# Kernel optimization log

Hardware: AMD Instinct MI355X
Metric: run time of the kernel (lower is better)

The kernel has to match this reference:

```python
import jax, jax.numpy as jnp
import numpy as np

B, T, C, H = 4096, 4, 1024, 8
DH = C // H
SCALE = DH ** -0.5
LN_EPS = 1e-5


def setup_inputs() -> dict:
    key = jax.random.key(0)
    k1, k2, k3 = jax.random.split(key, 3)
    feats = jax.random.normal(k1, (B, T, C), dtype=jnp.float32)
    Wqkv = jax.random.normal(k2, (T, C, 3 * C), dtype=jnp.float32) * 0.02
    bqkv = jnp.zeros((T, 3 * C), dtype=jnp.float32)
    Wproj = jax.random.normal(k3, (T, C, C), dtype=jnp.float32) * 0.02
    bproj = jnp.zeros((T, C), dtype=jnp.float32)
    gamma = jnp.ones((C,), dtype=jnp.float32)
    beta = jnp.zeros((C,), dtype=jnp.float32)
    return {"feats": feats, "Wqkv": Wqkv, "bqkv": bqkv,
            "Wproj": Wproj, "bproj": bproj, "gamma": gamma, "beta": beta}


def reference(feats, Wqkv, bqkv, Wproj, bproj, gamma, beta):
    # Grouped per-task QKV projection: [B,T,C] x [T,C,3C] -> [B,T,3C]
    qkv = jnp.einsum('btc,tcd->btd', feats, Wqkv) + bqkv
    q, k, v = jnp.split(qkv, 3, axis=-1)           # each [B,T,C]
    q = q.reshape(B, T, H, DH)
    k = k.reshape(B, T, H, DH)
    v = v.reshape(B, T, H, DH)
    # Cross-task attention: scores[b, query_task, key_task, head]
    scores = jnp.einsum('bqhd,bkhd->bqkh', q, k) * SCALE
    attn = jax.nn.softmax(scores, axis=2)          # softmax over key-task dim
    ctx = jnp.einsum('bqkh,bkhd->bqhd', attn, v)   # [B,T,H,DH]
    ctx = ctx.reshape(B, T, C)
    # Grouped per-task output projection (dropout is identity in eval)
    ctx = jnp.einsum('btc,tcd->btd', ctx, Wproj) + bproj
    # Residual + shared LayerNorm over channel dim
    x = ctx + feats
    mu = jnp.mean(x, axis=-1, keepdims=True)
    var = jnp.mean(jnp.square(x - mu), axis=-1, keepdims=True)
    return (x - mu) * jax.lax.rsqrt(var + LN_EPS) * gamma + beta
```

## Files before the change

kernel.cpp:

```cpp
#include <hip/hip_runtime.h>
#include <hip/hip_bf16.h>
#include <cstdint>
#include <cstddef>

#define B_SZ 4096
#define T_SZ 4
#define C_SZ 1024
#define H_SZ 8
#define DH_SZ 128
#define NQKV 3072
#define SCALE_F 0.08838834764831845f

typedef float f32x4 __attribute__((ext_vector_type(4)));
typedef short s16x8 __attribute__((ext_vector_type(8)));

static __device__ __forceinline__ float bf2f(unsigned short u) {
    union { unsigned int i; float f; } x; x.i = ((unsigned int)u) << 16; return x.f;
}
static __device__ __forceinline__ unsigned short f2bf(float f) {
    union { unsigned int i; float f; } x; x.f = f;
    unsigned int r = x.i + 0x7FFFu + ((x.i >> 16) & 1u);
    return (unsigned short)(r >> 16);
}

typedef const __attribute__((address_space(1))) void* gas_ptr;
typedef __attribute__((address_space(3))) void* las_ptr;
static __device__ __forceinline__ void async16(const void* g, void* l) {
    __builtin_amdgcn_global_load_lds((gas_ptr)g, (las_ptr)l, 16, 0, 0);
}

__global__ __launch_bounds__(256) void cvt_f32_bf16(const float* __restrict__ src,
                                                    unsigned short* __restrict__ dst, int n4) {
    int i = blockIdx.x * 256 + threadIdx.x;
    if (i >= n4) return;
    float4 v = reinterpret_cast<const float4*>(src)[i];
    ushort4 o;
    o.x = f2bf(v.x); o.y = f2bf(v.y); o.z = f2bf(v.z); o.w = f2bf(v.w);
    reinterpret_cast<ushort4*>(dst)[i] = o;
}

__global__ __launch_bounds__(256) void transpose_cvt(const float* __restrict__ src,
                                                     unsigned short* __restrict__ dst,
                                                     int K, int N) {
    __shared__ float tile[32][33];
    const float* s = src + (size_t)blockIdx.z * K * N;
    unsigned short* d = dst + (size_t)blockIdx.z * K * N;
    int n0 = blockIdx.x * 32, k0 = blockIdx.y * 32;
    int tx = threadIdx.x, ty = threadIdx.y;
#pragma unroll
    for (int i = 0; i < 4; i++) {
        int k = k0 + ty + i * 8;
        tile[ty + i * 8][tx] = s[(size_t)k * N + n0 + tx];
    }
    __syncthreads();
#pragma unroll
    for (int i = 0; i < 4; i++) {
        int n = n0 + ty + i * 8;
        d[(size_t)n * K + k0 + tx] = f2bf(tile[tx][ty + i * 8]);
    }
}

template<int NSIZE, int EPI>
__global__ __launch_bounds__(512, 1) void gemm256(
    const unsigned short* __restrict__ A,
    const unsigned short* __restrict__ Bt,
    const float* __restrict__ bias,
    const float* __restrict__ resid,
    unsigned short* __restrict__ out_bf,
    float* __restrict__ out_f)
{
    constexpr int BK  = 64;
    constexpr int NBX = NSIZE / 256;
    constexpr int NBY = B_SZ / 256;
    constexpr int NWG = NBX * NBY * T_SZ;

    __shared__ __align__(16) unsigned short lds[65536];

    const int bid = blockIdx.x;
    const int swz = (bid & 7) * (NWG >> 3) + (bid >> 3);
    const int by  = swz & (NBY - 1);
    const int tmp = swz >> 4;
    const int bx  = tmp % NBX;
    const int t   = tmp / NBX;
    const int m0  = by * 256;
    const int n0  = bx * 256;

    const int tid  = threadIdx.x;
    const int lane = tid & 63;
    const int w    = tid >> 6;
    const int wm   = w >> 2;
    const int wn   = w & 3;
    const int quad = lane >> 4;
    const int l16  = lane & 15;

    const int q0  = w * 128 + lane;
    const int q1  = q0 + 64;
    const int r0  = q0 >> 3, ch0 = (q0 & 7) ^ (r0 & 7);
    const int r1  = q1 >> 3, ch1 = (q1 & 7) ^ (r1 & 7);
    const unsigned short* Abase = A + (size_t)t * C_SZ;
    const unsigned short* Bbase = Bt + (size_t)t * NSIZE * C_SZ;
    const unsigned short* gA0 = Abase + (size_t)(m0 + r0) * (T_SZ * C_SZ) + ch0 * 8;
    const unsigned short* gA1 = Abase + (size_t)(m0 + r1) * (T_SZ * C_SZ) + ch1 * 8;
    const unsigned short* gB0 = Bbase + (size_t)(n0 + r0) * C_SZ + ch0 * 8;
    const unsigned short* gB1 = Bbase + (size_t)(n0 + r1) * C_SZ + ch1 * 8;
    unsigned short* dA0 = &lds[(w * 2 + 0) * 512];
    unsigned short* dA1 = &lds[(w * 2 + 1) * 512];
    unsigned short* dB0 = &lds[32768 + (w * 2 + 0) * 512];
    unsigned short* dB1 = &lds[32768 + (w * 2 + 1) * 512];

#define STG_A(buf, h, kt) do { \
    async16(gA0 + (size_t)(h) * 128 * (T_SZ * C_SZ) + (kt) * BK, dA0 + (buf) * 16384 + (h) * 8192); \
    async16(gA1 + (size_t)(h) * 128 * (T_SZ * C_SZ) + (kt) * BK, dA1 + (buf) * 16384 + (h) * 8192); \
} while (0)
#define STG_B(buf, h, kt) do { \
    async16(gB0 + (size_t)(h) * 128 * C_SZ + (kt) * BK, dB0 + (buf) * 16384 + (h) * 8192); \
    async16(gB1 + (size_t)(h) * 128 * C_SZ + (kt) * BK, dB1 + (buf) * 16384 + (h) * 8192); \
} while (0)

    const int s7   = l16 & 7;
    const int swk0 = ((0 * 4 + quad) ^ s7) * 8;
    const int swk1 = ((1 * 4 + quad) ^ s7) * 8;
    const unsigned short* aR = &lds[wm * 8192 + l16 * 64];
    const unsigned short* bR = &lds[32768 + (wn >> 1) * 8192 + ((wn & 1) * 64 + l16) * 64];

#define LD_A(buf, mh) do { \
    _Pragma("unroll") \
    for (int mi = 0; mi < 4; ++mi) { \
        af[mi][0] = *(const s16x8*)(aR + (buf) * 16384 + ((mh) * 4 + mi) * 1024 + swk0); \
        af[mi][1] = *(const s16x8*)(aR + (buf) * 16384 + ((mh) * 4 + mi) * 1024 + swk1); \
    } \
} while (0)
#define LD_B(buf, nh, dst) do { \
    _Pragma("unroll") \
    for (int ni = 0; ni < 2; ++ni) { \
        dst[ni][0] = *(const s16x8*)(bR + (buf) * 16384 + ((nh) * 2 + ni) * 1024 + swk0); \
        dst[ni][1] = *(const s16x8*)(bR + (buf) * 16384 + ((nh) * 2 + ni) * 1024 + swk1); \
    } \
} while (0)
#define MM(mh, nh, bsrc) do { \
    _Pragma("unroll") \
    for (int mi = 0; mi < 4; ++mi) \
    _Pragma("unroll") \
    for (int ni = 0; ni < 2; ++ni) { \
        acc[(mh) * 4 + mi][(nh) * 2 + ni] = __builtin_amdgcn_mfma_f32_16x16x32_bf16( \
            af[mi][0], bsrc[ni][0], acc[(mh) * 4 + mi][(nh) * 2 + ni], 0, 0, 0); \
        acc[(mh) * 4 + mi][(nh) * 2 + ni] = __builtin_amdgcn_mfma_f32_16x16x32_bf16( \
            af[mi][1], bsrc[ni][1], acc[(mh) * 4 + mi][(nh) * 2 + ni], 0, 0, 0); \
    } \
} while (0)
#define WAITK() do { \
    asm volatile("s_waitcnt lgkmcnt(0)"); \
    __builtin_amdgcn_sched_barrier(0); \
} while (0)
#define KTILE(buf, kt, SP0, SP23, VMC) do { \
     \
    asm volatile("s_waitcnt vmcnt(" #VMC ")"); \
    __builtin_amdgcn_sched_barrier(0); \
    __builtin_amdgcn_s_barrier(); \
    LD_A(buf, 0); LD_B(buf, 0, bq0); \
    if (SP0) STG_A((buf) ^ 1, 1, (kt) + 1); \
    WAITK(); \
    __builtin_amdgcn_s_setprio(1); MM(0, 0, bq0); __builtin_amdgcn_s_setprio(0); \
     \
    __builtin_amdgcn_s_barrier(); \
    LD_B(buf, 1, bq1); \
    WAITK(); \
    __builtin_amdgcn_s_setprio(1); MM(0, 1, bq1); __builtin_amdgcn_s_setprio(0); \
     \
    __builtin_amdgcn_s_barrier(); \
    LD_A(buf, 1); \
    if (SP23) { STG_B(buf, 0, (kt) + 2); STG_B(buf, 1, (kt) + 2); } \
    WAITK(); \
    __builtin_amdgcn_s_setprio(1); MM(1, 1, bq1); __builtin_amdgcn_s_setprio(0); \
     \
    __builtin_amdgcn_s_barrier(); \
    if (SP23) STG_A(buf, 0, (kt) + 2); \
    __builtin_amdgcn_s_setprio(1); MM(1, 0, bq0); __builtin_amdgcn_s_setprio(0); \
} while (0)

    f32x4 acc[8][4] = {};
    s16x8 af[4][2], bq0[2][2], bq1[2][2];

    STG_B(0, 0, 0); STG_B(0, 1, 0); STG_A(0, 0, 0); STG_A(0, 1, 0);
    STG_B(1, 0, 1); STG_B(1, 1, 1); STG_A(1, 0, 1);

#pragma clang loop unroll(disable)
    for (int it = 0; it < 7; ++it) {
        int kt = it * 2;
        KTILE(0, kt, 1, 1, 6);
        KTILE(1, kt + 1, 1, 1, 6);
    }
    KTILE(0, 14, 1, 0, 6);
    KTILE(1, 15, 0, 0, 0);

#undef KTILE
#undef WAITK
#undef MM
#undef LD_B
#undef LD_A
#undef STG_B
#undef STG_A

#pragma unroll
    for (int ni = 0; ni < 4; ++ni) {
        int gn = n0 + wn * 64 + ni * 16 + l16;
        float bi = bias[t * NSIZE + gn];
#pragma unroll
        for (int mi = 0; mi < 8; ++mi) {
#pragma unroll
            for (int r = 0; r < 4; ++r) {
                int gm = m0 + wm * 128 + mi * 16 + quad * 4 + r;
                size_t o = (size_t)(gm * T_SZ + t) * NSIZE + gn;
                float v = acc[mi][ni][r] + bi;
                if (EPI == 0) {
                    out_bf[o] = f2bf(v);
                } else {
                    out_f[o] = v + resid[o];
                }
            }
        }
    }
}

__global__ __launch_bounds__(256) void attn_kernel(const unsigned short* __restrict__ qkv,
                                                   unsigned short* __restrict__ ctx) {
    const int tid = threadIdx.x;
    const int li  = tid & 15;
    const int g   = blockIdx.x * 16 + (tid >> 4);
    const int b   = g >> 3, h = g & 7;
    const int d0  = li * 8;

    const unsigned short* base = qkv + (size_t)b * (T_SZ * NQKV) + h * DH_SZ + d0;
    float qf[4][8], kf[4][8], vf[4][8];
#pragma unroll
    for (int i = 0; i < 4; i++) {
        const unsigned short* p = base + (size_t)i * NQKV;
        s16x8 qv = *reinterpret_cast<const s16x8*>(p);
        s16x8 kv = *reinterpret_cast<const s16x8*>(p + C_SZ);
        s16x8 vv = *reinterpret_cast<const s16x8*>(p + 2 * C_SZ);
#pragma unroll
        for (int e = 0; e < 8; e++) {
            qf[i][e] = bf2f((unsigned short)qv[e]);
            kf[i][e] = bf2f((unsigned short)kv[e]);
            vf[i][e] = bf2f((unsigned short)vv[e]);
        }
    }
    float s[4][4];
#pragma unroll
    for (int i = 0; i < 4; i++)
#pragma unroll
        for (int j = 0; j < 4; j++) {
            float p = 0.0f;
#pragma unroll
            for (int e = 0; e < 8; e++) p += qf[i][e] * kf[j][e];
            p += __shfl_xor(p, 8);
            p += __shfl_xor(p, 4);
            p += __shfl_xor(p, 2);
            p += __shfl_xor(p, 1);
            s[i][j] = p * SCALE_F;
        }
#pragma unroll
    for (int i = 0; i < 4; i++) {
        float m = fmaxf(fmaxf(s[i][0], s[i][1]), fmaxf(s[i][2], s[i][3]));
        float e0 = __expf(s[i][0] - m), e1 = __expf(s[i][1] - m);
        float e2 = __expf(s[i][2] - m), e3 = __expf(s[i][3] - m);
        float inv = 1.0f / (e0 + e1 + e2 + e3);
        s[i][0] = e0 * inv; s[i][1] = e1 * inv; s[i][2] = e2 * inv; s[i][3] = e3 * inv;
    }
#pragma unroll
    for (int i = 0; i < 4; i++) {
        s16x8 ov;
#pragma unroll
        for (int e = 0; e < 8; e++) {
            float o = s[i][0] * vf[0][e] + s[i][1] * vf[1][e]
                    + s[i][2] * vf[2][e] + s[i][3] * vf[3][e];
            ov[e] = (short)f2bf(o);
        }
        *reinterpret_cast<s16x8*>(ctx + (size_t)(b * T_SZ + i) * C_SZ + h * DH_SZ + d0) = ov;
    }
}

__global__ __launch_bounds__(256) void ln_kernel(const float* __restrict__ y,
                                                 const float* __restrict__ gamma,
                                                 const float* __restrict__ beta,
                                                 float* __restrict__ out) {
    int row = blockIdx.x;
    int lane = threadIdx.x & 63, wave = threadIdx.x >> 6;
    float4 v = reinterpret_cast<const float4*>(y + (size_t)row * C_SZ)[threadIdx.x];
    float s  = v.x + v.y + v.z + v.w;
    float ss = v.x * v.x + v.y * v.y + v.z * v.z + v.w * v.w;
#pragma unroll
    for (int off = 32; off > 0; off >>= 1) { s += __shfl_xor(s, off); ss += __shfl_xor(ss, off); }
    __shared__ float red[8];
    if (lane == 0) { red[wave] = s; red[wave + 4] = ss; }
    __syncthreads();
    float S  = red[0] + red[1] + red[2] + red[3];
    float SS = red[4] + red[5] + red[6] + red[7];
    float mean = S * (1.0f / C_SZ);
    float var  = SS * (1.0f / C_SZ) - mean * mean;
    float inv  = rsqrtf(var + 1e-5f);
    float4 g  = reinterpret_cast<const float4*>(gamma)[threadIdx.x];
    float4 be = reinterpret_cast<const float4*>(beta)[threadIdx.x];
    float4 o;
    o.x = (v.x - mean) * inv * g.x + be.x;
    o.y = (v.y - mean) * inv * g.y + be.y;
    o.z = (v.z - mean) * inv * g.z + be.z;
    o.w = (v.w - mean) * inv * g.w + be.w;
    reinterpret_cast<float4*>(out + (size_t)row * C_SZ)[threadIdx.x] = o;
}

extern "C" void kernel_launch(void* const* d_in, const int* in_sizes, int n_in,
                              void* d_out, int out_size, void* d_ws, size_t ws_size,
                              hipStream_t stream) {
    const float* feats = (const float*)d_in[0];
    const float* Wqkv  = (const float*)d_in[1];
    const float* bqkv  = (const float*)d_in[2];
    const float* Wproj = (const float*)d_in[3];
    const float* bproj = (const float*)d_in[4];
    const float* gamma = (const float*)d_in[5];
    const float* beta  = (const float*)d_in[6];
    float* out = (float*)d_out;

    char* ws = (char*)d_ws;
    unsigned short* feats_bf = (unsigned short*)(ws);
    unsigned short* wqkv_t   = (unsigned short*)(ws + 33554432);
    unsigned short* wproj_t  = (unsigned short*)(ws + 58720256);
    unsigned short* qkv      = (unsigned short*)(ws + 67108864);
    unsigned short* ctx      = (unsigned short*)(ws + 167772160);
    float* ybuf              = (float*)(ws + 67108864);

    cvt_f32_bf16<<<16384, 256, 0, stream>>>(feats, feats_bf, (B_SZ * T_SZ * C_SZ) / 4);
    transpose_cvt<<<dim3(96, 32, 4), dim3(32, 8), 0, stream>>>(Wqkv, wqkv_t, C_SZ, NQKV);
    transpose_cvt<<<dim3(32, 32, 4), dim3(32, 8), 0, stream>>>(Wproj, wproj_t, C_SZ, C_SZ);

    gemm256<NQKV, 0><<<dim3(768), 512, 0, stream>>>(
        feats_bf, wqkv_t, bqkv, nullptr, qkv, nullptr);

    attn_kernel<<<(B_SZ * H_SZ) / 16, 256, 0, stream>>>(qkv, ctx);

    gemm256<C_SZ, 1><<<dim3(256), 512, 0, stream>>>(
        ctx, wproj_t, bproj, feats, nullptr, ybuf);

    ln_kernel<<<B_SZ * T_SZ, 256, 0, stream>>>(ybuf, gamma, beta, out);
}
```

Baseline: 417.8 us.

## Software-pipeline LDS fragment loads across k-tiles with double-buffered A registers

Restructures the GEMM k-loop so the LDS reads for the next k-tile's first A and B fragments are issued during the current tile's last MFMA phases. Two register buffers for A fragments (X/Y) rotate between tiles, and the explicit lgkmcnt waits are dropped in favour of barriers plus a single vmcnt wait per tile. This aims to hide LDS latency behind MFMA work, at the cost of more VGPRs and a reordered global staging schedule whose correctness depends on the barrier and vmcnt placement.

```diff
diff --git a/kernel.cpp b/kernel.cpp
--- a/kernel.cpp
+++ b/kernel.cpp
@@ -123,81 +123,85 @@
     const unsigned short* aR = &lds[wm * 8192 + l16 * 64];
     const unsigned short* bR = &lds[32768 + (wn >> 1) * 8192 + ((wn & 1) * 64 + l16) * 64];
 
-#define LD_A(buf, mh) do { \
+#define LD_An(bufi, mh, DST) do { \
     _Pragma("unroll") \
     for (int mi = 0; mi < 4; ++mi) { \
-        af[mi][0] = *(const s16x8*)(aR + (buf) * 16384 + ((mh) * 4 + mi) * 1024 + swk0); \
-        af[mi][1] = *(const s16x8*)(aR + (buf) * 16384 + ((mh) * 4 + mi) * 1024 + swk1); \
+        DST[mi][0] = *(const s16x8*)(aR + (bufi) * 16384 + ((mh) * 4 + mi) * 1024 + swk0); \
+        DST[mi][1] = *(const s16x8*)(aR + (bufi) * 16384 + ((mh) * 4 + mi) * 1024 + swk1); \
     } \
 } while (0)
-#define LD_B(buf, nh, dst) do { \
+#define LD_Bn(bufi, nh, DST) do { \
     _Pragma("unroll") \
     for (int ni = 0; ni < 2; ++ni) { \
-        dst[ni][0] = *(const s16x8*)(bR + (buf) * 16384 + ((nh) * 2 + ni) * 1024 + swk0); \
-        dst[ni][1] = *(const s16x8*)(bR + (buf) * 16384 + ((nh) * 2 + ni) * 1024 + swk1); \
+        DST[ni][0] = *(const s16x8*)(bR + (bufi) * 16384 + ((nh) * 2 + ni) * 1024 + swk0); \
+        DST[ni][1] = *(const s16x8*)(bR + (bufi) * 16384 + ((nh) * 2 + ni) * 1024 + swk1); \
     } \
 } while (0)
-#define MM(mh, nh, bsrc) do { \
+#define MMn(AARR, mh, nh, BARR) do { \
     _Pragma("unroll") \
     for (int mi = 0; mi < 4; ++mi) \
     _Pragma("unroll") \
     for (int ni = 0; ni < 2; ++ni) { \
         acc[(mh) * 4 + mi][(nh) * 2 + ni] = __builtin_amdgcn_mfma_f32_16x16x32_bf16( \
-            af[mi][0], bsrc[ni][0], acc[(mh) * 4 + mi][(nh) * 2 + ni], 0, 0, 0); \
+            AARR[mi][0], BARR[ni][0], acc[(mh) * 4 + mi][(nh) * 2 + ni], 0, 0, 0); \
         acc[(mh) * 4 + mi][(nh) * 2 + ni] = __builtin_amdgcn_mfma_f32_16x16x32_bf16( \
-            af[mi][1], bsrc[ni][1], acc[(mh) * 4 + mi][(nh) * 2 + ni], 0, 0, 0); \
+            AARR[mi][1], BARR[ni][1], acc[(mh) * 4 + mi][(nh) * 2 + ni], 0, 0, 0); \
     } \
 } while (0)
-#define WAITK() do { \
-    asm volatile("s_waitcnt lgkmcnt(0)"); \
+#define SBAR() do { \
+    __builtin_amdgcn_s_barrier(); \
     __builtin_amdgcn_sched_barrier(0); \
 } while (0)
-#define KTILE(buf, kt, SP0, SP23, VMC) do { \
+#define KTILE(buf, kt, P, Q, SP0, SPB0, SPP3, RDN, VM2) do { \
      \
-    asm volatile("s_waitcnt vmcnt(" #VMC ")"); \
+    SBAR(); \
+    LD_An(buf, 1, Q); \
+    if (SP0) STG_A((buf) ^ 1, 1, (kt) + 1); \
+    __builtin_amdgcn_s_setprio(1); MMn(P, 0, 0, b0); __builtin_amdgcn_s_setprio(0); \
+     \
+    SBAR(); \
+    LD_Bn(buf, 1, b1); \
+    __builtin_amdgcn_s_setprio(1); MMn(Q, 1, 0, b0); __builtin_amdgcn_s_setprio(0); \
+     \
+    if (VM2) { asm volatile("s_waitcnt vmcnt(0)"); } \
     __builtin_amdgcn_sched_barrier(0); \
-    __builtin_amdgcn_s_barrier(); \
-    LD_A(buf, 0); LD_B(buf, 0, bq0); \
-    if (SP0) STG_A((buf) ^ 1, 1, (kt) + 1); \
-    WAITK(); \
-    __builtin_amdgcn_s_setprio(1); MM(0, 0, bq0); __builtin_amdgcn_s_setprio(0); \
+    SBAR(); \
+    __builtin_amdgcn_s_setprio(1); MMn(Q, 1, 1, b1); __builtin_amdgcn_s_setprio(0); \
+    if (RDN) LD_An((buf) ^ 1, 0, Q); \
+    if (SPB0) STG_B(buf, 0, (kt) + 2); \
      \
-    __builtin_amdgcn_s_barrier(); \
-    LD_B(buf, 1, bq1); \
-    WAITK(); \
-    __builtin_amdgcn_s_setprio(1); MM(0, 1, bq1); __builtin_amdgcn_s_setprio(0); \
-     \
-    __builtin_amdgcn_s_barrier(); \
-    LD_A(buf, 1); \
-    if (SP23) { STG_B(buf, 0, (kt) + 2); STG_B(buf, 1, (kt) + 2); } \
-    WAITK(); \
-    __builtin_amdgcn_s_setprio(1); MM(1, 1, bq1); __builtin_amdgcn_s_setprio(0); \
-     \
-    __builtin_amdgcn_s_barrier(); \
-    if (SP23) STG_A(buf, 0, (kt) + 2); \
-    __builtin_amdgcn_s_setprio(1); MM(1, 0, bq0); __builtin_amdgcn_s_setprio(0); \
+    SBAR(); \
+    if (RDN) LD_Bn((buf) ^ 1, 0, b0); \
+    if (SPP3) { STG_A(buf, 0, (kt) + 2); STG_B(buf, 1, (kt) + 2); } \
+    __builtin_amdgcn_s_setprio(1); MMn(P, 0, 1, b1); __builtin_amdgcn_s_setprio(0); \
 } while (0)
 
     f32x4 acc[8][4] = {};
-    s16x8 af[4][2], bq0[2][2], bq1[2][2];
-
-    STG_B(0, 0, 0); STG_B(0, 1, 0); STG_A(0, 0, 0); STG_A(0, 1, 0);
-    STG_B(1, 0, 1); STG_B(1, 1, 1); STG_A(1, 0, 1);
+    s16x8 X[4][2], Y[4][2], b0[2][2], b1[2][2];
+
+    STG_A(0, 0, 0); STG_A(0, 1, 0); STG_B(0, 0, 0); STG_B(0, 1, 0);
+    asm volatile("s_waitcnt vmcnt(0)");
+    __builtin_amdgcn_sched_barrier(0);
+    SBAR();
+    LD_An(0, 0, X);
+    LD_Bn(0, 0, b0);
+    STG_B(1, 0, 1);
+    STG_A(1, 0, 1); STG_B(1, 1, 1);
 
 #pragma clang loop unroll(disable)
     for (int it = 0; it < 7; ++it) {
         int kt = it * 2;
-        KTILE(0, kt, 1, 1, 6);
-        KTILE(1, kt + 1, 1, 1, 6);
-    }
-    KTILE(0, 14, 1, 0, 6);
-    KTILE(1, 15, 0, 0, 0);
+        KTILE(0, kt,     X, Y, 1, 1, 1, 1, 1);
+        KTILE(1, kt + 1, Y, X, 1, 1, 1, 1, 1);
+    }
+    KTILE(0, 14, X, Y, 1, 0, 0, 1, 1);
+    KTILE(1, 15, Y, X, 0, 0, 0, 0, 0);
 
 #undef KTILE
-#undef WAITK
-#undef MM
-#undef LD_B
-#undef LD_A
+#undef SBAR
+#undef MMn
+#undef LD_Bn
+#undef LD_An
 #undef STG_B
 #undef STG_A
 
```

After: 442.4 us. 5.9% more time.

## Merge GEMM K-tile phases from four barriers to two, dropping explicit LDS waits

Applied to the files above, without the earlier changes.

Restructures each K-tile of the MFMA GEMM mainloop from four barrier-separated phases to two. Both B fragments and the first A fragment are loaded together, and the explicit lgkmcnt waits are removed so the compiler inserts the waits itself. Global-to-LDS staging is reordered to match, with all three next-stage stores issued in the second phase. This reduces barrier and wait overhead and lets LDS reads overlap the MFMAs. In exchange it holds more registers live, and correctness now depends on the compiler's implicit waits and on the tighter reuse of the LDS buffers.

```diff
diff --git a/kernel.cpp b/kernel.cpp
--- a/kernel.cpp
+++ b/kernel.cpp
@@ -148,53 +148,45 @@
             af[mi][1], bsrc[ni][1], acc[(mh) * 4 + mi][(nh) * 2 + ni], 0, 0, 0); \
     } \
 } while (0)
-#define WAITK() do { \
-    asm volatile("s_waitcnt lgkmcnt(0)"); \
+#define WALL() do { \
+    __builtin_amdgcn_s_barrier(); \
     __builtin_amdgcn_sched_barrier(0); \
 } while (0)
 #define KTILE(buf, kt, SP0, SP23, VMC) do { \
      \
     asm volatile("s_waitcnt vmcnt(" #VMC ")"); \
     __builtin_amdgcn_sched_barrier(0); \
-    __builtin_amdgcn_s_barrier(); \
-    LD_A(buf, 0); LD_B(buf, 0, bq0); \
+    WALL(); \
+    LD_B(buf, 0, bq0); \
+    LD_A(buf, 0); \
+    LD_B(buf, 1, bq1); \
     if (SP0) STG_A((buf) ^ 1, 1, (kt) + 1); \
-    WAITK(); \
-    __builtin_amdgcn_s_setprio(1); MM(0, 0, bq0); __builtin_amdgcn_s_setprio(0); \
+    __builtin_amdgcn_s_setprio(1); MM(0, 0, bq0); MM(0, 1, bq1); __builtin_amdgcn_s_setprio(0); \
      \
-    __builtin_amdgcn_s_barrier(); \
-    LD_B(buf, 1, bq1); \
-    WAITK(); \
-    __builtin_amdgcn_s_setprio(1); MM(0, 1, bq1); __builtin_amdgcn_s_setprio(0); \
-     \
-    __builtin_amdgcn_s_barrier(); \
+    WALL(); \
     LD_A(buf, 1); \
-    if (SP23) { STG_B(buf, 0, (kt) + 2); STG_B(buf, 1, (kt) + 2); } \
-    WAITK(); \
-    __builtin_amdgcn_s_setprio(1); MM(1, 1, bq1); __builtin_amdgcn_s_setprio(0); \
-     \
-    __builtin_amdgcn_s_barrier(); \
-    if (SP23) STG_A(buf, 0, (kt) + 2); \
-    __builtin_amdgcn_s_setprio(1); MM(1, 0, bq0); __builtin_amdgcn_s_setprio(0); \
+    if (SP23) { STG_B(buf, 0, (kt) + 2); STG_A(buf, 0, (kt) + 2); STG_B(buf, 1, (kt) + 2); } \
+    __builtin_amdgcn_s_setprio(1); MM(1, 1, bq1); MM(1, 0, bq0); __builtin_amdgcn_s_setprio(0); \
 } while (0)
 
     f32x4 acc[8][4] = {};
     s16x8 af[4][2], bq0[2][2], bq1[2][2];
 
-    STG_B(0, 0, 0); STG_B(0, 1, 0); STG_A(0, 0, 0); STG_A(0, 1, 0);
-    STG_B(1, 0, 1); STG_B(1, 1, 1); STG_A(1, 0, 1);
+    STG_A(0, 0, 0); STG_B(0, 0, 0); STG_B(0, 1, 0);
+    STG_A(0, 1, 0);
+    STG_B(1, 0, 1); STG_A(1, 0, 1); STG_B(1, 1, 1);
 
 #pragma clang loop unroll(disable)
     for (int it = 0; it < 7; ++it) {
         int kt = it * 2;
-        KTILE(0, kt, 1, 1, 6);
+        KTILE(0, kt,     1, 1, 6);
         KTILE(1, kt + 1, 1, 1, 6);
     }
     KTILE(0, 14, 1, 0, 6);
     KTILE(1, 15, 0, 0, 0);
 
 #undef KTILE
-#undef WAITK
+#undef WALL
 #undef MM
 #undef LD_B
 #undef LD_A
```

Measured after the change: 405.4 us. -3.0%, faster.
